# Performance work log

Hardware: AMD Instinct MI355X
Metric: run time of the kernel (lower is better)

Reference implementation:

```python
import jax, jax.numpy as jnp
import numpy as np

N = 2000        # num_genes (nodes)
E = 64000       # edges
Q = 200000      # query edges
F_IN = 512      # num_features
H = 64          # hidden
Q_PHASE = 0.25  # magnetic charge q
SIM_DIM = 64
LABELS = 2


def _msconv(xr, xi, src, dst, w, W, n):
    """MagNet/MSGNN Chebyshev conv, K=1, sym normalization, absolute degree.

    A_s = (A + A^T)/2, Theta_ij = 2*pi*q*(A_ij - A_ji),
    L_hat = L - I = -D^{-1/2} A_s D^{-1/2} * exp(i*Theta)  (lambda_max = 2)
    out = X @ W[0] + (L_hat X) @ W[1]   (real weights on complex signal)
    """
    # symmetrize: each directed edge contributes entries (src->dst) and (dst->src)
    ss = jnp.concatenate([src, dst])
    dd = jnp.concatenate([dst, src])
    ws = jnp.concatenate([w, w]) * 0.5
    theta = 2.0 * jnp.pi * Q_PHASE * jnp.concatenate([w, -w])
    # absolute degree of symmetrized adjacency
    deg = jax.ops.segment_sum(jnp.abs(ws), dd, num_segments=n)
    dinv = jnp.where(deg > 0, 1.0 / jnp.sqrt(deg), 0.0)
    norm = ws * dinv[ss] * dinv[dd]
    cr = -norm * jnp.cos(theta)  # real part of L_hat entries
    ci = -norm * jnp.sin(theta)  # imag part
    xrs, xis = xr[ss], xi[ss]
    t1r = jax.ops.segment_sum(cr[:, None] * xrs - ci[:, None] * xis, dd, num_segments=n)
    t1i = jax.ops.segment_sum(cr[:, None] * xis + ci[:, None] * xrs, dd, num_segments=n)
    return xr @ W[0] + t1r @ W[1], xi @ W[0] + t1i @ W[1]


def setup_inputs() -> dict:
    key = jax.random.key(0)
    ks = jax.random.split(key, 10)
    real = jax.random.normal(ks[0], (N, F_IN), jnp.float32)
    imag = jax.random.normal(ks[1], (N, F_IN), jnp.float32)
    edge_index = jax.random.randint(ks[2], (2, E), 0, N, dtype=jnp.int64)
    query_edges = jax.random.randint(ks[3], (Q, 2), 0, N, dtype=jnp.int64)
    all_embeddings = jax.random.normal(ks[4], (N * N, SIM_DIM), jnp.float32)
    edge_weight = jax.random.uniform(ks[5], (E,), jnp.float32)
    W1 = jax.random.normal(ks[6], (2, F_IN, H), jnp.float32) / np.sqrt(F_IN)
    W2 = jax.random.normal(ks[7], (2, H, H), jnp.float32) / np.sqrt(H)
    lin_w = jax.random.normal(ks[8], (4 * H + SIM_DIM, LABELS), jnp.float32) * 0.05
    lin_b = jnp.zeros((LABELS,), jnp.float32)
    return {"real": real, "imag": imag, "edge_index": edge_index,
            "query_edges": query_edges, "all_embeddings": all_embeddings,
            "edge_weight": edge_weight, "W1": W1, "W2": W2,
            "lin_w": lin_w, "lin_b": lin_b}


def reference(real, imag, edge_index, query_edges, all_embeddings, edge_weight,
              W1, W2, lin_w, lin_b):
    src, dst = edge_index[0], edge_index[1]
    for W in (W1, W2):
        real, imag = _msconv(real, imag, src, dst, edge_weight, W, N)
        mask = (real >= 0).astype(real.dtype)   # complex_relu
        real = real * mask
        imag = imag * mask
    ni, nj = query_edges[:, 0], query_edges[:, 1]
    sim = all_embeddings[ni * N + nj]           # vectorized per-edge lookup
    x = jnp.concatenate([real[ni], real[nj], imag[ni], imag[nj], sim], axis=-1)
    # eval mode: dropout is identity
    logits = x @ lin_w + lin_b
    return jax.nn.log_softmax(logits, axis=1)
```

## Files before the change

### kernel.cpp

```cpp
#include <hip/hip_runtime.h>
#include <math.h>

constexpr int N_NODES = 2000;
constexpr int F_IN    = 512;
constexpr int H_DIM   = 64;
constexpr int SLOT_SH = 8;

__global__ __launch_bounds__(256) void deg_kernel(
    const int* __restrict__ ei, const float* __restrict__ w,
    float* __restrict__ deg, int E)
{
  int e = blockIdx.x * 256 + threadIdx.x;
  if (e >= E) return;
  int s = ei[e], d = ei[E + e];
  float aw = fabsf(0.5f * w[e]);
  atomicAdd(&deg[d], aw);
  atomicAdd(&deg[s], aw);
}

__global__ __launch_bounds__(256) void build_slots_kernel(
    const int* __restrict__ ei, const float* __restrict__ w,
    const float* __restrict__ deg, int* __restrict__ cnt,
    int* __restrict__ nbr, float* __restrict__ cra, float* __restrict__ cia, int E)
{
  int e = blockIdx.x * 256 + threadIdx.x;
  if (e >= E) return;
  int s = ei[e], d = ei[E + e];
  float ww = w[e];
  float degs = deg[s], degd = deg[d];
  float dvs = (degs > 0.f) ? rsqrtf(degs) : 0.f;
  float dvd = (degd > 0.f) ? rsqrtf(degd) : 0.f;
  float norm = 0.5f * ww * dvs * dvd;
  float sn, cs;
  sincosf(1.5707963267948966f * ww, &sn, &cs);
  float cr = -norm * cs;
  float ci = -norm * sn;
  int p1 = atomicAdd(&cnt[d], 1);
  int i1 = (d << SLOT_SH) + p1;
  nbr[i1] = s; cra[i1] = cr; cia[i1] = ci;
  int p2 = atomicAdd(&cnt[s], 1);
  int i2 = (s << SLOT_SH) + p2;
  nbr[i2] = d; cra[i2] = cr; cia[i2] = -ci;
}

__global__ __launch_bounds__(256) void gemm_kernel(
    const float* __restrict__ Ar, const float* __restrict__ Ai,
    const float* __restrict__ Wb,
    float* __restrict__ P0r, float* __restrict__ P0i,
    float* __restrict__ P1r, float* __restrict__ P1i,
    int M, int K, int accumulate)
{
  __shared__ float As[64][65];
  __shared__ float Ws[64][64];
  int t = threadIdx.x;
  int which = blockIdx.y;
  const float* A = (which & 1) ? Ai : Ar;
  const float* W = Wb + (size_t)(which >> 1) * K * H_DIM;
  float* C = (which == 0) ? P0r : (which == 1) ? P0i : (which == 2) ? P1r : P1i;
  int r0 = blockIdx.x * 64;
  int kchunk = K / gridDim.z;
  int kbeg = blockIdx.z * kchunk;
  int kend = kbeg + kchunk;
  int tx = t & 15, ty = t >> 4;
  float acc[4][4] = {};
  for (int k0 = kbeg; k0 < kend; k0 += 64) {
    #pragma unroll
    for (int i = 0; i < 16; i++) {
      int idx = t + i * 256;
      int row = idx >> 6, kk = idx & 63;
      int gr = r0 + row;
      As[row][kk] = (gr < M) ? A[(size_t)gr * K + k0 + kk] : 0.f;
    }
    #pragma unroll
    for (int i = 0; i < 16; i++) {
      int idx = t + i * 256;
      int kk = idx >> 6, col = idx & 63;
      Ws[kk][col] = W[(size_t)(k0 + kk) * H_DIM + col];
    }
    __syncthreads();
    #pragma unroll
    for (int kk = 0; kk < 64; kk++) {
      float4 wv = *reinterpret_cast<const float4*>(&Ws[kk][tx * 4]);
      float av[4];
      #pragma unroll
      for (int r = 0; r < 4; r++) av[r] = As[ty * 4 + r][kk];
      #pragma unroll
      for (int r = 0; r < 4; r++) {
        acc[r][0] = fmaf(av[r], wv.x, acc[r][0]);
        acc[r][1] = fmaf(av[r], wv.y, acc[r][1]);
        acc[r][2] = fmaf(av[r], wv.z, acc[r][2]);
        acc[r][3] = fmaf(av[r], wv.w, acc[r][3]);
      }
    }
    __syncthreads();
  }
  #pragma unroll
  for (int r = 0; r < 4; r++) {
    int gr = r0 + ty * 4 + r;
    if (gr >= M) continue;
    size_t o = (size_t)gr * H_DIM + tx * 4;
    if (accumulate) {
      atomicAdd(&C[o + 0], acc[r][0]);
      atomicAdd(&C[o + 1], acc[r][1]);
      atomicAdd(&C[o + 2], acc[r][2]);
      atomicAdd(&C[o + 3], acc[r][3]);
    } else {
      *reinterpret_cast<float4*>(&C[o]) =
          make_float4(acc[r][0], acc[r][1], acc[r][2], acc[r][3]);
    }
  }
}

__global__ __launch_bounds__(256) void aggregate1_kernel(
    const int* __restrict__ cnt, const int* __restrict__ nbr,
    const float* __restrict__ cra, const float* __restrict__ cia,
    const float* __restrict__ P0r, const float* __restrict__ P0i,
    const float* __restrict__ P1r, const float* __restrict__ P1i,
    float* __restrict__ xr, float* __restrict__ xi)
{
  __shared__ float sr[4][64], si[4][64];
  int v = blockIdx.x;
  int h = threadIdx.x & 63;
  int wv = threadIdx.x >> 6;
  int cv = cnt[v];
  float ar = 0.f, ai = 0.f;
  for (int j = wv; j < cv; j += 4) {
    int idx = (v << SLOT_SH) + j;
    int u = nbr[idx];
    float cr = cra[idx], ci = cia[idx];
    float pr = P1r[u * H_DIM + h];
    float pi = P1i[u * H_DIM + h];
    ar = fmaf(cr, pr, ar); ar = fmaf(-ci, pi, ar);
    ai = fmaf(cr, pi, ai); ai = fmaf( ci, pr, ai);
  }
  sr[wv][h] = ar; si[wv][h] = ai;
  __syncthreads();
  if (wv == 0) {
    ar = sr[0][h] + sr[1][h] + sr[2][h] + sr[3][h] + P0r[v * H_DIM + h];
    ai = si[0][h] + si[1][h] + si[2][h] + si[3][h] + P0i[v * H_DIM + h];
    if (ar < 0.f) { ar = 0.f; ai = 0.f; }
    xr[v * H_DIM + h] = ar;
    xi[v * H_DIM + h] = ai;
  }
}

__global__ __launch_bounds__(256) void aggregate2_kernel(
    const int* __restrict__ cnt, const int* __restrict__ nbr,
    const float* __restrict__ cra, const float* __restrict__ cia,
    const float* __restrict__ P0r, const float* __restrict__ P0i,
    const float* __restrict__ P1r, const float* __restrict__ P1i,
    const float* __restrict__ lw, const float* __restrict__ lb,
    float4* __restrict__ node_uw)
{
  __shared__ float sr[4][64], si[4][64];
  int v = blockIdx.x;
  int h = threadIdx.x & 63;
  int wv = threadIdx.x >> 6;
  int cv = cnt[v];
  float ar = 0.f, ai = 0.f;
  for (int j = wv; j < cv; j += 4) {
    int idx = (v << SLOT_SH) + j;
    int u = nbr[idx];
    float cr = cra[idx], ci = cia[idx];
    float pr = P1r[u * H_DIM + h];
    float pi = P1i[u * H_DIM + h];
    ar = fmaf(cr, pr, ar); ar = fmaf(-ci, pi, ar);
    ai = fmaf(cr, pi, ai); ai = fmaf( ci, pr, ai);
  }
  sr[wv][h] = ar; si[wv][h] = ai;
  __syncthreads();
  if (wv == 0) {
    ar = sr[0][h] + sr[1][h] + sr[2][h] + sr[3][h] + P0r[v * H_DIM + h];
    ai = si[0][h] + si[1][h] + si[2][h] + si[3][h] + P0i[v * H_DIM + h];
    if (ar < 0.f) { ar = 0.f; ai = 0.f; }
    const float2* lw2 = reinterpret_cast<const float2*>(lw);
    float2 l0 = lw2[h], l1 = lw2[64 + h], l2 = lw2[128 + h], l3 = lw2[192 + h];
    float u0 = ar * l0.x + ai * l2.x;
    float u1 = ar * l0.y + ai * l2.y;
    float w0 = ar * l1.x + ai * l3.x;
    float w1 = ar * l1.y + ai * l3.y;
    #pragma unroll
    for (int off = 1; off < 64; off <<= 1) {
      u0 += __shfl_xor(u0, off, 64);
      u1 += __shfl_xor(u1, off, 64);
      w0 += __shfl_xor(w0, off, 64);
      w1 += __shfl_xor(w1, off, 64);
    }
    if (h == 0)
      node_uw[v] = make_float4(u0 + lb[0], u1 + lb[1], w0, w1);
  }
}

__global__ __launch_bounds__(256) void query_kernel(
    const int* __restrict__ qe,
    const float* __restrict__ emb,
    const float* __restrict__ lw,
    const float4* __restrict__ node_uw,
    float* __restrict__ out, int Qn, int n)
{
  int gq = (blockIdx.x * 256 + threadIdx.x) >> 4;
  int l  = threadIdx.x & 15;
  if (gq >= Qn) return;
  int ni = qe[2 * gq], nj = qe[2 * gq + 1];
  const float4* emb4 = reinterpret_cast<const float4*>(emb);
  float4 s4 = emb4[(size_t)(ni * n + nj) * 16 + l];
  const float2* lw2 = reinterpret_cast<const float2*>(lw);
  float2 wa = lw2[256 + 4 * l];
  float2 wb = lw2[257 + 4 * l];
  float2 wc = lw2[258 + 4 * l];
  float2 wd = lw2[259 + 4 * l];
  float acc0 = s4.x * wa.x + s4.y * wb.x + s4.z * wc.x + s4.w * wd.x;
  float acc1 = s4.x * wa.y + s4.y * wb.y + s4.z * wc.y + s4.w * wd.y;
  #pragma unroll
  for (int off = 1; off < 16; off <<= 1) {
    acc0 += __shfl_xor(acc0, off, 64);
    acc1 += __shfl_xor(acc1, off, 64);
  }
  if (l == 0) {
    float4 uni = node_uw[ni];
    float4 unj = node_uw[nj];
    float lg0 = acc0 + uni.x + unj.z;
    float lg1 = acc1 + uni.y + unj.w;
    float m = fmaxf(lg0, lg1);
    float lse = m + logf(expf(lg0 - m) + expf(lg1 - m));
    reinterpret_cast<float2*>(out)[gq] = make_float2(lg0 - lse, lg1 - lse);
  }
}

extern "C" void kernel_launch(void* const* d_in, const int* in_sizes, int n_in,
                              void* d_out, int out_size, void* d_ws, size_t ws_size,
                              hipStream_t stream)
{
  const float* real = (const float*)d_in[0];
  const float* imag = (const float*)d_in[1];
  const int*   ei   = (const int*)d_in[2];
  const int*   qe   = (const int*)d_in[3];
  const float* emb  = (const float*)d_in[4];
  const float* ew   = (const float*)d_in[5];
  const float* W1   = (const float*)d_in[6];
  const float* W2   = (const float*)d_in[7];
  const float* lw   = (const float*)d_in[8];
  const float* lb   = (const float*)d_in[9];
  float* out = (float*)d_out;

  int E = in_sizes[2] / 2;
  int Q = in_sizes[3] / 2;
  int n = N_NODES;
  int nslots = N_NODES << SLOT_SH;

  char* ws = (char*)d_ws;
  size_t off = 0;
  auto alloc = [&](size_t bytes) -> char* {
    char* p = ws + off;
    off = (off + bytes + 255) & ~(size_t)255;
    return p;
  };
  float*  deg  = (float*) alloc(2048 * 4);
  int*    cnt  = (int*)   alloc(2048 * 4);
  float*  P0r  = (float*) alloc((size_t)n * H_DIM * 4);
  float*  P0i  = (float*) alloc((size_t)n * H_DIM * 4);
  float*  P1r  = (float*) alloc((size_t)n * H_DIM * 4);
  float*  P1i  = (float*) alloc((size_t)n * H_DIM * 4);
  size_t zero_bytes = (size_t)((char*)(P1i + (size_t)n * H_DIM) - (char*)deg);
  int*    nbr  = (int*)   alloc((size_t)nslots * 4);
  float*  cra  = (float*) alloc((size_t)nslots * 4);
  float*  cia  = (float*) alloc((size_t)nslots * 4);
  float*  xr1  = (float*) alloc((size_t)n * H_DIM * 4);
  float*  xi1  = (float*) alloc((size_t)n * H_DIM * 4);
  float4* nuw  = (float4*)alloc((size_t)n * 16);

  hipMemsetAsync(deg, 0, zero_bytes, stream);

  int eb = (E + 255) / 256;
  deg_kernel<<<eb, 256, 0, stream>>>(ei, ew, deg, E);
  build_slots_kernel<<<eb, 256, 0, stream>>>(ei, ew, deg, cnt, nbr, cra, cia, E);

  dim3 g1((n + 63) / 64, 4, 2);
  gemm_kernel<<<g1, 256, 0, stream>>>(real, imag, W1, P0r, P0i, P1r, P1i, n, F_IN, 1);
  aggregate1_kernel<<<n, 256, 0, stream>>>(cnt, nbr, cra, cia,
                                           P0r, P0i, P1r, P1i, xr1, xi1);
  dim3 g2((n + 63) / 64, 4, 1);
  gemm_kernel<<<g2, 256, 0, stream>>>(xr1, xi1, W2, P0r, P0i, P1r, P1i, n, H_DIM, 0);
  aggregate2_kernel<<<n, 256, 0, stream>>>(cnt, nbr, cra, cia,
                                           P0r, P0i, P1r, P1i, lw, lb, nuw);

  query_kernel<<<(Q * 16 + 255) / 256, 256, 0, stream>>>(qe, emb, lw, nuw, out, Q, n);
}
```

Baseline: 140.5 us.

## Fuse degree/slot build with layer-1 GEMM and defer normalization to aggregation

```diff
diff --git a/kernel.cpp b/kernel.cpp
--- a/kernel.cpp
+++ b/kernel.cpp
@@ -3,79 +3,30 @@
 
 constexpr int N_NODES = 2000;
 constexpr int F_IN    = 512;
-constexpr int H_DIM   = 64;
+constexpr int H       = 64;
 constexpr int SLOT_SH = 8;
 
-__global__ __launch_bounds__(256) void deg_kernel(
-    const int* __restrict__ ei, const float* __restrict__ w,
-    float* __restrict__ deg, int E)
-{
-  int e = blockIdx.x * 256 + threadIdx.x;
-  if (e >= E) return;
-  int s = ei[e], d = ei[E + e];
-  float aw = fabsf(0.5f * w[e]);
-  atomicAdd(&deg[d], aw);
-  atomicAdd(&deg[s], aw);
-}
-
-__global__ __launch_bounds__(256) void build_slots_kernel(
-    const int* __restrict__ ei, const float* __restrict__ w,
-    const float* __restrict__ deg, int* __restrict__ cnt,
-    int* __restrict__ nbr, float* __restrict__ cra, float* __restrict__ cia, int E)
-{
-  int e = blockIdx.x * 256 + threadIdx.x;
-  if (e >= E) return;
-  int s = ei[e], d = ei[E + e];
-  float ww = w[e];
-  float degs = deg[s], degd = deg[d];
-  float dvs = (degs > 0.f) ? rsqrtf(degs) : 0.f;
-  float dvd = (degd > 0.f) ? rsqrtf(degd) : 0.f;
-  float norm = 0.5f * ww * dvs * dvd;
-  float sn, cs;
-  sincosf(1.5707963267948966f * ww, &sn, &cs);
-  float cr = -norm * cs;
-  float ci = -norm * sn;
-  int p1 = atomicAdd(&cnt[d], 1);
-  int i1 = (d << SLOT_SH) + p1;
-  nbr[i1] = s; cra[i1] = cr; cia[i1] = ci;
-  int p2 = atomicAdd(&cnt[s], 1);
-  int i2 = (s << SLOT_SH) + p2;
-  nbr[i2] = d; cra[i2] = cr; cia[i2] = -ci;
-}
-
-__global__ __launch_bounds__(256) void gemm_kernel(
-    const float* __restrict__ Ar, const float* __restrict__ Ai,
-    const float* __restrict__ Wb,
-    float* __restrict__ P0r, float* __restrict__ P0i,
-    float* __restrict__ P1r, float* __restrict__ P1i,
-    int M, int K, int accumulate)
-{
-  __shared__ float As[64][65];
-  __shared__ float Ws[64][64];
-  int t = threadIdx.x;
-  int which = blockIdx.y;
-  const float* A = (which & 1) ? Ai : Ar;
-  const float* W = Wb + (size_t)(which >> 1) * K * H_DIM;
-  float* C = (which == 0) ? P0r : (which == 1) ? P0i : (which == 2) ? P1r : P1i;
-  int r0 = blockIdx.x * 64;
-  int kchunk = K / gridDim.z;
-  int kbeg = blockIdx.z * kchunk;
-  int kend = kbeg + kchunk;
+__device__ __forceinline__ void gemm_tile256(
+    const float* __restrict__ A, const float* __restrict__ W,
+    float (*As)[65], float (*Ws)[64],
+    int r0, int K, float* __restrict__ C)
+{
+  int t  = threadIdx.x;
   int tx = t & 15, ty = t >> 4;
   float acc[4][4] = {};
-  for (int k0 = kbeg; k0 < kend; k0 += 64) {
+  for (int k0 = 0; k0 < K; k0 += 64) {
     #pragma unroll
     for (int i = 0; i < 16; i++) {
       int idx = t + i * 256;
       int row = idx >> 6, kk = idx & 63;
       int gr = r0 + row;
-      As[row][kk] = (gr < M) ? A[(size_t)gr * K + k0 + kk] : 0.f;
+      As[row][kk] = (gr < N_NODES) ? A[(size_t)gr * K + k0 + kk] : 0.f;
     }
     #pragma unroll
     for (int i = 0; i < 16; i++) {
       int idx = t + i * 256;
       int kk = idx >> 6, col = idx & 63;
-      Ws[kk][col] = W[(size_t)(k0 + kk) * H_DIM + col];
+      Ws[kk][col] = W[(size_t)(k0 + kk) * H + col];
     }
     __syncthreads();
     #pragma unroll
@@ -97,81 +48,143 @@
   #pragma unroll
   for (int r = 0; r < 4; r++) {
     int gr = r0 + ty * 4 + r;
-    if (gr >= M) continue;
-    size_t o = (size_t)gr * H_DIM + tx * 4;
-    if (accumulate) {
-      atomicAdd(&C[o + 0], acc[r][0]);
-      atomicAdd(&C[o + 1], acc[r][1]);
-      atomicAdd(&C[o + 2], acc[r][2]);
-      atomicAdd(&C[o + 3], acc[r][3]);
-    } else {
-      *reinterpret_cast<float4*>(&C[o]) =
+    if (gr < N_NODES) {
+      *reinterpret_cast<float4*>(&C[(size_t)gr * H + tx * 4]) =
           make_float4(acc[r][0], acc[r][1], acc[r][2], acc[r][3]);
     }
   }
 }
 
-__global__ __launch_bounds__(256) void aggregate1_kernel(
+__global__ __launch_bounds__(256) void fused1_kernel(
+    const float* __restrict__ real, const float* __restrict__ imag,
+    const float* __restrict__ W1,
+    const int* __restrict__ ei, const float* __restrict__ ew,
+    float* __restrict__ deg, int* __restrict__ cnt,
+    int* __restrict__ nbr, float* __restrict__ cra, float* __restrict__ cia,
+    float* __restrict__ P0r, float* __restrict__ P0i,
+    float* __restrict__ P1r, float* __restrict__ P1i, int E)
+{
+  __shared__ float As[64][65];
+  __shared__ float Ws[64][64];
+  if (blockIdx.x < 128) {
+    int bi = blockIdx.x;
+    int which = bi & 3, tile = bi >> 2;
+    const float* A = (which & 1) ? imag : real;
+    const float* W = W1 + (size_t)(which >> 1) * F_IN * H;
+    float* C = (which == 0) ? P0r : (which == 1) ? P0i
+             : (which == 2) ? P1r : P1i;
+    gemm_tile256(A, W, As, Ws, tile * 64, F_IN, C);
+  } else {
+    int e = (blockIdx.x - 128) * 256 + threadIdx.x;
+    if (e < E) {
+      int s = ei[e], d = ei[E + e];
+      float ww = ew[e];
+      float aw = fabsf(0.5f * ww);
+      atomicAdd(&deg[d], aw);
+      atomicAdd(&deg[s], aw);
+      float sn, cs;
+      sincosf(1.5707963267948966f * ww, &sn, &cs);
+      float cr = -0.5f * ww * cs;
+      float ci = -0.5f * ww * sn;
+      int p1 = atomicAdd(&cnt[d], 1);
+      int i1 = (d << SLOT_SH) + p1;
+      nbr[i1] = s; cra[i1] = cr; cia[i1] = ci;
+      int p2 = atomicAdd(&cnt[s], 1);
+      int i2 = (s << SLOT_SH) + p2;
+      nbr[i2] = d; cra[i2] = cr; cia[i2] = -ci;
+    }
+  }
+}
+
+__device__ __forceinline__ void agg_partial(
     const int* __restrict__ cnt, const int* __restrict__ nbr,
     const float* __restrict__ cra, const float* __restrict__ cia,
-    const float* __restrict__ P0r, const float* __restrict__ P0i,
-    const float* __restrict__ P1r, const float* __restrict__ P1i,
-    float* __restrict__ xr, float* __restrict__ xi)
-{
-  __shared__ float sr[4][64], si[4][64];
-  int v = blockIdx.x;
-  int h = threadIdx.x & 63;
-  int wv = threadIdx.x >> 6;
+    const float* __restrict__ deg,
+    const float* __restrict__ Pr, const float* __restrict__ Pi,
+    int v, int h, int wv, float& aro, float& aio)
+{
   int cv = cnt[v];
   float ar = 0.f, ai = 0.f;
   for (int j = wv; j < cv; j += 4) {
     int idx = (v << SLOT_SH) + j;
     int u = nbr[idx];
-    float cr = cra[idx], ci = cia[idx];
-    float pr = P1r[u * H_DIM + h];
-    float pi = P1i[u * H_DIM + h];
+    float dg = deg[u];
+    float du = (dg > 0.f) ? rsqrtf(dg) : 0.f;
+    float cr = cra[idx] * du, ci = cia[idx] * du;
+    float pr = Pr[u * H + h];
+    float pi = Pi[u * H + h];
     ar = fmaf(cr, pr, ar); ar = fmaf(-ci, pi, ar);
     ai = fmaf(cr, pi, ai); ai = fmaf( ci, pr, ai);
   }
-  sr[wv][h] = ar; si[wv][h] = ai;
-  __syncthreads();
-  if (wv == 0) {
-    ar = sr[0][h] + sr[1][h] + sr[2][h] + sr[3][h] + P0r[v * H_DIM + h];
-    ai = si[0][h] + si[1][h] + si[2][h] + si[3][h] + P0i[v * H_DIM + h];
-    if (ar < 0.f) { ar = 0.f; ai = 0.f; }
-    xr[v * H_DIM + h] = ar;
-    xi[v * H_DIM + h] = ai;
-  }
-}
-
-__global__ __launch_bounds__(256) void aggregate2_kernel(
+  aro = ar; aio = ai;
+}
+
+__global__ __launch_bounds__(256) void aggregate1_kernel(
     const int* __restrict__ cnt, const int* __restrict__ nbr,
     const float* __restrict__ cra, const float* __restrict__ cia,
+    const float* __restrict__ deg,
     const float* __restrict__ P0r, const float* __restrict__ P0i,
     const float* __restrict__ P1r, const float* __restrict__ P1i,
-    const float* __restrict__ lw, const float* __restrict__ lb,
-    float4* __restrict__ node_uw)
+    float* __restrict__ xr, float* __restrict__ xi)
 {
   __shared__ float sr[4][64], si[4][64];
   int v = blockIdx.x;
   int h = threadIdx.x & 63;
   int wv = threadIdx.x >> 6;
-  int cv = cnt[v];
-  float ar = 0.f, ai = 0.f;
-  for (int j = wv; j < cv; j += 4) {
-    int idx = (v << SLOT_SH) + j;
-    int u = nbr[idx];
-    float cr = cra[idx], ci = cia[idx];
-    float pr = P1r[u * H_DIM + h];
-    float pi = P1i[u * H_DIM + h];
-    ar = fmaf(cr, pr, ar); ar = fmaf(-ci, pi, ar);
-    ai = fmaf(cr, pi, ai); ai = fmaf( ci, pr, ai);
-  }
+  float ar, ai;
+  agg_partial(cnt, nbr, cra, cia, deg, P1r, P1i, v, h, wv, ar, ai);
   sr[wv][h] = ar; si[wv][h] = ai;
   __syncthreads();
   if (wv == 0) {
-    ar = sr[0][h] + sr[1][h] + sr[2][h] + sr[3][h] + P0r[v * H_DIM + h];
-    ai = si[0][h] + si[1][h] + si[2][h] + si[3][h] + P0i[v * H_DIM + h];
+    float dgv = deg[v];
+    float dv = (dgv > 0.f) ? rsqrtf(dgv) : 0.f;
+    ar = (sr[0][h] + sr[1][h] + sr[2][h] + sr[3][h]) * dv + P0r[v * H + h];
+    ai = (si[0][h] + si[1][h] + si[2][h] + si[3][h]) * dv + P0i[v * H + h];
+    if (ar < 0.f) { ar = 0.f; ai = 0.f; }
+    xr[v * H + h] = ar;
+    xi[v * H + h] = ai;
+  }
+}
+
+__global__ __launch_bounds__(256) void gemm2_kernel(
+    const float* __restrict__ xr, const float* __restrict__ xi,
+    const float* __restrict__ W2,
+    float* __restrict__ P0r, float* __restrict__ P0i,
+    float* __restrict__ P1r, float* __restrict__ P1i)
+{
+  __shared__ float As[64][65];
+  __shared__ float Ws[64][64];
+  int bi = blockIdx.x;
+  int which = bi & 3, tile = bi >> 2;
+  const float* A = (which & 1) ? xi : xr;
+  const float* W = W2 + (size_t)(which >> 1) * H * H;
+  float* C = (which == 0) ? P0r : (which == 1) ? P0i
+           : (which == 2) ? P1r : P1i;
+  gemm_tile256(A, W, As, Ws, tile * 64, H, C);
+}
+
+__global__ __launch_bounds__(256) void aggregate2_kernel(
+    const int* __restrict__ cnt, const int* __restrict__ nbr,
+    const float* __restrict__ cra, const float* __restrict__ cia,
+    const float* __restrict__ deg,
+    const float* __restrict__ P0r, const float* __restrict__ P0i,
+    const float* __restrict__ P1r, const float* __restrict__ P1i,
+    const float* __restrict__ lw, const float* __restrict__ lb,
+    float4* __restrict__ nuw)
+{
+  __shared__ float sr[4][64], si[4][64];
+  int v = blockIdx.x;
+  int h = threadIdx.x & 63;
+  int wv = threadIdx.x >> 6;
+  float ar, ai;
+  agg_partial(cnt, nbr, cra, cia, deg, P1r, P1i, v, h, wv, ar, ai);
+  sr[wv][h] = ar; si[wv][h] = ai;
+  __syncthreads();
+  if (wv == 0) {
+    float dgv = deg[v];
+    float dv = (dgv > 0.f) ? rsqrtf(dgv) : 0.f;
+    ar = (sr[0][h] + sr[1][h] + sr[2][h] + sr[3][h]) * dv + P0r[v * H + h];
+    ai = (si[0][h] + si[1][h] + si[2][h] + si[3][h]) * dv + P0i[v * H + h];
     if (ar < 0.f) { ar = 0.f; ai = 0.f; }
     const float2* lw2 = reinterpret_cast<const float2*>(lw);
     float2 l0 = lw2[h], l1 = lw2[64 + h], l2 = lw2[128 + h], l3 = lw2[192 + h];
@@ -187,43 +200,61 @@
       w1 += __shfl_xor(w1, off, 64);
     }
     if (h == 0)
-      node_uw[v] = make_float4(u0 + lb[0], u1 + lb[1], w0, w1);
+      nuw[v] = make_float4(u0 + lb[0], u1 + lb[1], w0, w1);
   }
 }
 
 __global__ __launch_bounds__(256) void query_kernel(
-    const int* __restrict__ qe,
-    const float* __restrict__ emb,
-    const float* __restrict__ lw,
-    const float4* __restrict__ node_uw,
-    float* __restrict__ out, int Qn, int n)
-{
-  int gq = (blockIdx.x * 256 + threadIdx.x) >> 4;
-  int l  = threadIdx.x & 15;
-  if (gq >= Qn) return;
-  int ni = qe[2 * gq], nj = qe[2 * gq + 1];
-  const float4* emb4 = reinterpret_cast<const float4*>(emb);
-  float4 s4 = emb4[(size_t)(ni * n + nj) * 16 + l];
+    const int* __restrict__ qe, const float* __restrict__ emb,
+    const float* __restrict__ lw, const float4* __restrict__ nuw,
+    float2* __restrict__ out, int Qn, int n)
+{
   const float2* lw2 = reinterpret_cast<const float2*>(lw);
+  int l = threadIdx.x & 15;
   float2 wa = lw2[256 + 4 * l];
   float2 wb = lw2[257 + 4 * l];
   float2 wc = lw2[258 + 4 * l];
   float2 wd = lw2[259 + 4 * l];
-  float acc0 = s4.x * wa.x + s4.y * wb.x + s4.z * wc.x + s4.w * wd.x;
-  float acc1 = s4.x * wa.y + s4.y * wb.y + s4.z * wc.y + s4.w * wd.y;
-  #pragma unroll
-  for (int off = 1; off < 16; off <<= 1) {
-    acc0 += __shfl_xor(acc0, off, 64);
-    acc1 += __shfl_xor(acc1, off, 64);
-  }
-  if (l == 0) {
-    float4 uni = node_uw[ni];
-    float4 unj = node_uw[nj];
-    float lg0 = acc0 + uni.x + unj.z;
-    float lg1 = acc1 + uni.y + unj.w;
-    float m = fmaxf(lg0, lg1);
-    float lse = m + logf(expf(lg0 - m) + expf(lg1 - m));
-    reinterpret_cast<float2*>(out)[gq] = make_float2(lg0 - lse, lg1 - lse);
+  int g0 = (blockIdx.x * 256 + threadIdx.x) >> 4;
+  int ng = (gridDim.x * 256) >> 4;
+  const float4* emb4 = reinterpret_cast<const float4*>(emb);
+  for (int q = g0; q < Qn; q += 2 * ng) {
+    int q2 = q + ng;
+    bool has2 = q2 < Qn;
+    int ni0 = qe[2 * q], nj0 = qe[2 * q + 1];
+    int ni1 = has2 ? qe[2 * q2] : ni0;
+    int nj1 = has2 ? qe[2 * q2 + 1] : nj0;
+    float4 sa = emb4[((size_t)ni0 * n + nj0) * 16 + l];
+    float4 sb = emb4[((size_t)ni1 * n + nj1) * 16 + l];
+    float a0 = sa.x * wa.x + sa.y * wb.x + sa.z * wc.x + sa.w * wd.x;
+    float a1 = sa.x * wa.y + sa.y * wb.y + sa.z * wc.y + sa.w * wd.y;
+    float b0 = sb.x * wa.x + sb.y * wb.x + sb.z * wc.x + sb.w * wd.x;
+    float b1 = sb.x * wa.y + sb.y * wb.y + sb.z * wc.y + sb.w * wd.y;
+    #pragma unroll
+    for (int off = 1; off < 16; off <<= 1) {
+      a0 += __shfl_xor(a0, off, 64);
+      a1 += __shfl_xor(a1, off, 64);
+      b0 += __shfl_xor(b0, off, 64);
+      b1 += __shfl_xor(b1, off, 64);
+    }
+    if (l == 0) {
+      float4 uni = nuw[ni0];
+      float4 unj = nuw[nj0];
+      float lg0 = a0 + uni.x + unj.z;
+      float lg1 = a1 + uni.y + unj.w;
+      float m = fmaxf(lg0, lg1);
+      float lse = m + logf(expf(lg0 - m) + expf(lg1 - m));
+      out[q] = make_float2(lg0 - lse, lg1 - lse);
+      if (has2) {
+        float4 uni2 = nuw[ni1];
+        float4 unj2 = nuw[nj1];
+        float mg0 = b0 + uni2.x + unj2.z;
+        float mg1 = b1 + uni2.y + unj2.w;
+        float m2 = fmaxf(mg0, mg1);
+        float lse2 = m2 + logf(expf(mg0 - m2) + expf(mg1 - m2));
+        out[q2] = make_float2(mg0 - lse2, mg1 - lse2);
+      }
+    }
   }
 }
 
@@ -241,7 +272,7 @@
   const float* W2   = (const float*)d_in[7];
   const float* lw   = (const float*)d_in[8];
   const float* lb   = (const float*)d_in[9];
-  float* out = (float*)d_out;
+  float2* out = (float2*)d_out;
 
   int E = in_sizes[2] / 2;
   int Q = in_sizes[3] / 2;
@@ -255,34 +286,29 @@
     off = (off + bytes + 255) & ~(size_t)255;
     return p;
   };
-  float*  deg  = (float*) alloc(2048 * 4);
-  int*    cnt  = (int*)   alloc(2048 * 4);
-  float*  P0r  = (float*) alloc((size_t)n * H_DIM * 4);
-  float*  P0i  = (float*) alloc((size_t)n * H_DIM * 4);
-  float*  P1r  = (float*) alloc((size_t)n * H_DIM * 4);
-  float*  P1i  = (float*) alloc((size_t)n * H_DIM * 4);
-  size_t zero_bytes = (size_t)((char*)(P1i + (size_t)n * H_DIM) - (char*)deg);
-  int*    nbr  = (int*)   alloc((size_t)nslots * 4);
-  float*  cra  = (float*) alloc((size_t)nslots * 4);
-  float*  cia  = (float*) alloc((size_t)nslots * 4);
-  float*  xr1  = (float*) alloc((size_t)n * H_DIM * 4);
-  float*  xi1  = (float*) alloc((size_t)n * H_DIM * 4);
-  float4* nuw  = (float4*)alloc((size_t)n * 16);
-
-  hipMemsetAsync(deg, 0, zero_bytes, stream);
-
-  int eb = (E + 255) / 256;
-  deg_kernel<<<eb, 256, 0, stream>>>(ei, ew, deg, E);
-  build_slots_kernel<<<eb, 256, 0, stream>>>(ei, ew, deg, cnt, nbr, cra, cia, E);
-
-  dim3 g1((n + 63) / 64, 4, 2);
-  gemm_kernel<<<g1, 256, 0, stream>>>(real, imag, W1, P0r, P0i, P1r, P1i, n, F_IN, 1);
-  aggregate1_kernel<<<n, 256, 0, stream>>>(cnt, nbr, cra, cia,
+  float*  deg = (float*)alloc(2048 * 4);
+  int*    cnt = (int*)  alloc(2048 * 4);
+  int*    nbr = (int*)  alloc((size_t)nslots * 4);
+  float*  cra = (float*)alloc((size_t)nslots * 4);
+  float*  cia = (float*)alloc((size_t)nslots * 4);
+  float*  P0r = (float*)alloc((size_t)n * H * 4);
+  float*  P0i = (float*)alloc((size_t)n * H * 4);
+  float*  P1r = (float*)alloc((size_t)n * H * 4);
+  float*  P1i = (float*)alloc((size_t)n * H * 4);
+  float*  xr1 = (float*)alloc((size_t)n * H * 4);
+  float*  xi1 = (float*)alloc((size_t)n * H * 4);
+  float4* nuw = (float4*)alloc((size_t)n * 16);
+
+  hipMemsetAsync(deg, 0, 2 * 2048 * 4, stream);
+
+  int eblocks = (E + 255) / 256;
+  fused1_kernel<<<128 + eblocks, 256, 0, stream>>>(
+      real, imag, W1, ei, ew, deg, cnt, nbr, cra, cia,
+      P0r, P0i, P1r, P1i, E);
+  aggregate1_kernel<<<n, 256, 0, stream>>>(cnt, nbr, cra, cia, deg,
                                            P0r, P0i, P1r, P1i, xr1, xi1);
-  dim3 g2((n + 63) / 64, 4, 1);
-  gemm_kernel<<<g2, 256, 0, stream>>>(xr1, xi1, W2, P0r, P0i, P1r, P1i, n, H_DIM, 0);
-  aggregate2_kernel<<<n, 256, 0, stream>>>(cnt, nbr, cra, cia,
+  gemm2_kernel<<<128, 256, 0, stream>>>(xr1, xi1, W2, P0r, P0i, P1r, P1i);
+  aggregate2_kernel<<<n, 256, 0, stream>>>(cnt, nbr, cra, cia, deg,
                                            P0r, P0i, P1r, P1i, lw, lb, nuw);
-
-  query_kernel<<<(Q * 16 + 255) / 256, 256, 0, stream>>>(qe, emb, lw, nuw, out, Q, n);
-}
+  query_kernel<<<2048, 256, 0, stream>>>(qe, emb, lw, nuw, out, Q, n);
+}
```

Result: slower. 144.4 us (+2.8%).
